# Optimization experiments

Measured on AMD Instinct MI355X. Metric: run time of the kernel, lower is better.

## Reference

```python
import jax, jax.numpy as jnp
import numpy as np

D_MODEL = 1024
NUM_HEADS = 16
D_K = D_MODEL // NUM_HEADS
B, S = 2, 2048


def setup_inputs() -> dict:
    key = jax.random.key(0)
    ks = jax.random.split(key, 11)
    s = 1.0 / np.sqrt(D_MODEL)
    inp = {
        "Q": jax.random.normal(ks[0], (B, S, D_MODEL), jnp.float32),
        "K": jax.random.normal(ks[1], (B, S, D_MODEL), jnp.float32),
        "V": jax.random.normal(ks[2], (B, S, D_MODEL), jnp.float32),
        "Wq": jax.random.uniform(ks[3], (D_MODEL, D_MODEL), jnp.float32, -s, s),
        "bq": jax.random.uniform(ks[4], (D_MODEL,), jnp.float32, -s, s),
        "Wk": jax.random.uniform(ks[5], (D_MODEL, D_MODEL), jnp.float32, -s, s),
        "bk": jax.random.uniform(ks[6], (D_MODEL,), jnp.float32, -s, s),
        "Wv": jax.random.uniform(ks[7], (D_MODEL, D_MODEL), jnp.float32, -s, s),
        "bv": jax.random.uniform(ks[8], (D_MODEL,), jnp.float32, -s, s),
        "Wo": jax.random.uniform(ks[9], (D_MODEL, D_MODEL), jnp.float32, -s, s),
        "bo": jax.random.uniform(ks[10], (D_MODEL,), jnp.float32, -s, s),
    }
    return inp


def _split_heads(x):
    b, s, _ = x.shape
    return x.reshape(b, s, NUM_HEADS, D_K).transpose(0, 2, 1, 3)  # [B,H,S,Dk]


def reference(Q, K, V, Wq, bq, Wk, bk, Wv, bv, Wo, bo):
    q = _split_heads(Q @ Wq.T + bq)
    k = _split_heads(K @ Wk.T + bk)
    v = _split_heads(V @ Wv.T + bv)
    scale = 1.0 / jnp.sqrt(jnp.asarray(D_K, q.dtype))
    scores = jnp.einsum("bhqd,bhkd->bhqk", q, k) * scale  # [B,H,S,S]
    attn = jax.nn.softmax(scores, axis=-1)
    out = jnp.einsum("bhqk,bhkd->bhqd", attn, v)
    out = out.transpose(0, 2, 1, 3).reshape(Q.shape[0], -1, D_MODEL)
    return out @ Wo.T + bo
```

## Files before the change

kernel.cpp:

```cpp
#include <hip/hip_runtime.h>
#include <stdint.h>

typedef __bf16 bf16;
typedef __bf16 bf16x8 __attribute__((ext_vector_type(8)));
typedef float floatx4 __attribute__((ext_vector_type(4)));

#define S_LEN 2048
#define DM 1024
#define NH 16
#define DK 64
#define MTOT 4096

__device__ __forceinline__ void gll16(const void* g, void* l) {
  __builtin_amdgcn_global_load_lds(
      (const __attribute__((address_space(1))) void*)g,
      (__attribute__((address_space(3))) void*)l, 16, 0, 0);
}

__global__ __launch_bounds__(256) void cvt_kernel(
    const float* __restrict__ Wq, const float* __restrict__ Wk, const float* __restrict__ Wv,
    const float* __restrict__ Xq, const float* __restrict__ Xk,
    bf16* __restrict__ wqb, bf16* __restrict__ wkb, bf16* __restrict__ wvb,
    bf16* __restrict__ xqb, bf16* __restrict__ xkb)
{
  const int c = blockIdx.x;
  const float* src; bf16* dst; int off;
  if      (c < 512)  { src = Wq; dst = wqb; off = c; }
  else if (c < 1024) { src = Wk; dst = wkb; off = c - 512; }
  else if (c < 1536) { src = Wv; dst = wvb; off = c - 1024; }
  else if (c < 3584) { src = Xq; dst = xqb; off = c - 1536; }
  else               { src = Xk; dst = xkb; off = c - 3584; }
  const size_t base = (size_t)off * 2048 + threadIdx.x * 8;
  float4 a = *(const float4*)(src + base);
  float4 b = *(const float4*)(src + base + 4);
  bf16x8 h;
  h[0] = (bf16)a.x; h[1] = (bf16)a.y; h[2] = (bf16)a.z; h[3] = (bf16)a.w;
  h[4] = (bf16)b.x; h[5] = (bf16)b.y; h[6] = (bf16)b.z; h[7] = (bf16)b.w;
  *(bf16x8*)(dst + base) = h;
}

__global__ __launch_bounds__(256) void proj_kernel(
    const bf16* __restrict__ xqb, const bf16* __restrict__ xkb, const float* __restrict__ Xv,
    const bf16* __restrict__ wqb, const bf16* __restrict__ wkb, const bf16* __restrict__ wvb,
    const float* __restrict__ bqp, const float* __restrict__ bkp, const float* __restrict__ bvp,
    bf16* __restrict__ qb, bf16* __restrict__ kb, bf16* __restrict__ vtb)
{
  const int z = blockIdx.z;
  const bf16* W     = (z == 0) ? wqb : (z == 1) ? wkb : wvb;
  const float* bias = (z == 0) ? bqp : (z == 1) ? bkp : bvp;

  const int m0 = blockIdx.x * 128;
  const int n0 = blockIdx.y * 128;
  const int tid = threadIdx.x;
  const int lane = tid & 63;
  const int wid = tid >> 6;
  const int wm = (wid & 1) * 64;
  const int wn = (wid >> 1) * 64;

  __shared__ unsigned char smemA[32768];
  __shared__ bf16 Bs[128 * 64];
  bf16*  As16 = (bf16*)smemA;
  float* Asf  = (float*)smemA;

  floatx4 acc[4][4];
  #pragma unroll
  for (int i = 0; i < 4; i++)
    #pragma unroll
    for (int j = 0; j < 4; j++) acc[i][j] = (floatx4){0.f, 0.f, 0.f, 0.f};

  const int mr = lane & 15;
  const int q4 = lane >> 4;

  const int r8_in = lane >> 3, cb8_ph = lane & 7;
  const int r4_in = lane >> 4, cb16_ph = lane & 15;

  const bf16* Xb = (z == 0) ? xqb : xkb;

  for (int kt = 0; kt < DM; kt += 64) {
    __syncthreads();
    if (z < 2) {
      #pragma unroll
      for (int j = 0; j < 4; j++) {
        const int c = wid * 4 + j;
        const int row = c * 8 + r8_in;
        const int cb = cb8_ph ^ (row & 7);
        gll16(Xb + (size_t)(m0 + row) * DM + kt + cb * 8, &As16[c * 512]);
      }
    } else {
      #pragma unroll
      for (int j = 0; j < 8; j++) {
        const int c = wid * 8 + j;
        const int row = c * 4 + r4_in;
        const int cb = cb16_ph ^ (row & 7);
        gll16(Xv + (size_t)(m0 + row) * DM + kt + cb * 4, &Asf[c * 256]);
      }
    }
    #pragma unroll
    for (int j = 0; j < 4; j++) {
      const int c = wid * 4 + j;
      const int row = c * 8 + r8_in;
      const int cb = cb8_ph ^ (row & 7);
      gll16(W + (size_t)(n0 + row) * DM + kt + cb * 8, &Bs[c * 512]);
    }
    __syncthreads();

    #pragma unroll
    for (int kk = 0; kk < 2; kk++) {
      bf16x8 af[4], bfr[4];
      #pragma unroll
      for (int mt = 0; mt < 4; mt++) {
        const int row = wm + mt * 16 + mr;
        if (z < 2) {
          const int cb = 4 * kk + q4;
          af[mt] = *(const bf16x8*)&As16[row * 64 + (cb ^ (row & 7)) * 8];
        } else {
          const int cb0 = 8 * kk + 2 * q4;
          const float4 lo = *(const float4*)&Asf[row * 64 + (cb0 ^ (row & 7)) * 4];
          const float4 hi = *(const float4*)&Asf[row * 64 + ((cb0 + 1) ^ (row & 7)) * 4];
          bf16x8 a;
          a[0] = (bf16)lo.x; a[1] = (bf16)lo.y; a[2] = (bf16)lo.z; a[3] = (bf16)lo.w;
          a[4] = (bf16)hi.x; a[5] = (bf16)hi.y; a[6] = (bf16)hi.z; a[7] = (bf16)hi.w;
          af[mt] = a;
        }
      }
      #pragma unroll
      for (int nt = 0; nt < 4; nt++) {
        const int row = wn + nt * 16 + mr;
        const int cb = 4 * kk + q4;
        bfr[nt] = *(const bf16x8*)&Bs[row * 64 + (cb ^ (row & 7)) * 8];
      }
      #pragma unroll
      for (int mt = 0; mt < 4; mt++)
        #pragma unroll
        for (int nt = 0; nt < 4; nt++)
          acc[mt][nt] = __builtin_amdgcn_mfma_f32_16x16x32_bf16(af[mt], bfr[nt], acc[mt][nt], 0, 0, 0);
    }
  }

  const float qscale = (z == 0) ? 0.125f : 1.0f;
  #pragma unroll
  for (int nt = 0; nt < 4; nt++) {
    const int gn = n0 + wn + nt * 16 + mr;
    const float bv = bias[gn];
    const int h = gn >> 6, d = gn & 63;
    #pragma unroll
    for (int mt = 0; mt < 4; mt++) {
      const int mbase = m0 + wm + mt * 16 + q4 * 4;
      #pragma unroll
      for (int r = 0; r < 4; r++) {
        const int gm = mbase + r;
        const int bi = gm >> 11, s = gm & 2047;
        const bf16 hv = (bf16)((acc[mt][nt][r] + bv) * qscale);
        if (z == 2) {
          vtb[(((size_t)(bi * NH + h)) * DK + d) * S_LEN + s] = hv;
        } else if (z == 0) {
          qb[(((size_t)(bi * NH + h)) * S_LEN + s) * DK + d] = hv;
        } else {
          kb[(((size_t)(bi * NH + h)) * S_LEN + s) * DK + d] = hv;
        }
      }
    }
  }
}

__global__ __launch_bounds__(256) void attn_kernel(
    const bf16* __restrict__ qb, const bf16* __restrict__ kb,
    const bf16* __restrict__ vtb, bf16* __restrict__ ob)
{
  const int qt = blockIdx.x;
  const int bh = blockIdx.y;
  const int tid = threadIdx.x;
  const int lane = tid & 63;
  const int wid = tid >> 6;

  const bf16* qh = qb + (size_t)bh * S_LEN * DK;
  const bf16* kh = kb + (size_t)bh * S_LEN * DK;
  const bf16* vh = vtb + (size_t)bh * DK * S_LEN;

  __shared__ bf16 Ks[128 * 64];
  __shared__ bf16 Vs[64 * 128];
  __shared__ bf16 Ps[4][32][136];

  const int mr = lane & 15;
  const int q4 = lane >> 4;

  bf16x8 aq[2][2];
  #pragma unroll
  for (int mt = 0; mt < 2; mt++)
    #pragma unroll
    for (int kk = 0; kk < 2; kk++)
      aq[mt][kk] = *(const bf16x8*)(qh + (size_t)(qt * 128 + wid * 32 + mt * 16 + mr) * DK + kk * 32 + q4 * 8);

  floatx4 acc_o[2][4];
  #pragma unroll
  for (int mt = 0; mt < 2; mt++)
    #pragma unroll
    for (int dt = 0; dt < 4; dt++) acc_o[mt][dt] = (floatx4){0.f, 0.f, 0.f, 0.f};
  float l_p[2][4] = {{0.f,0.f,0.f,0.f},{0.f,0.f,0.f,0.f}};

  const int r8_in = lane >> 3, cb8_ph = lane & 7;
  const int r4_in = lane >> 4, cb16_ph = lane & 15;

  for (int it = 0; it < S_LEN / 128; it++) {
    const int s0 = it * 128;
    __syncthreads();
    #pragma unroll
    for (int j = 0; j < 4; j++) {
      const int c = wid * 4 + j;
      const int row = c * 8 + r8_in;
      const int cb = cb8_ph ^ (row & 7);
      gll16(kh + (size_t)(s0 + row) * DK + cb * 8, &Ks[c * 512]);
    }
    #pragma unroll
    for (int j = 0; j < 4; j++) {
      const int c = wid * 4 + j;
      const int row = c * 4 + r4_in;
      const int cb = cb16_ph ^ (row & 7);
      gll16(vh + (size_t)row * S_LEN + s0 + cb * 8, &Vs[c * 512]);
    }
    __syncthreads();

    floatx4 sc[2][8];
    #pragma unroll
    for (int mt = 0; mt < 2; mt++)
      #pragma unroll
      for (int i = 0; i < 8; i++) sc[mt][i] = (floatx4){0.f, 0.f, 0.f, 0.f};
    #pragma unroll
    for (int kk = 0; kk < 2; kk++) {
      #pragma unroll
      for (int nt = 0; nt < 8; nt++) {
        const int row = nt * 16 + mr;
        const int cb = kk * 4 + q4;
        bf16x8 b = *(const bf16x8*)&Ks[row * 64 + (cb ^ (row & 7)) * 8];
        #pragma unroll
        for (int mt = 0; mt < 2; mt++)
          sc[mt][nt] = __builtin_amdgcn_mfma_f32_16x16x32_bf16(aq[mt][kk], b, sc[mt][nt], 0, 0, 0);
      }
    }

    #pragma unroll
    for (int mt = 0; mt < 2; mt++)
      #pragma unroll
      for (int nt = 0; nt < 8; nt++)
        #pragma unroll
        for (int r = 0; r < 4; r++) {
          const float pv = __expf(sc[mt][nt][r]);
          l_p[mt][r] += pv;
          Ps[wid][mt * 16 + q4 * 4 + r][nt * 16 + mr] = (bf16)pv;
        }

    #pragma unroll
    for (int kk2 = 0; kk2 < 4; kk2++) {
      bf16x8 ap[2];
      #pragma unroll
      for (int mt = 0; mt < 2; mt++)
        ap[mt] = *(const bf16x8*)&Ps[wid][mt * 16 + mr][kk2 * 32 + q4 * 8];
      #pragma unroll
      for (int dt = 0; dt < 4; dt++) {
        const int row = dt * 16 + mr;
        const int cb = kk2 * 4 + q4;
        bf16x8 b = *(const bf16x8*)&Vs[row * 128 + (cb ^ (row & 7)) * 8];
        #pragma unroll
        for (int mt = 0; mt < 2; mt++)
          acc_o[mt][dt] = __builtin_amdgcn_mfma_f32_16x16x32_bf16(ap[mt], b, acc_o[mt][dt], 0, 0, 0);
      }
    }
  }

  const int bi = bh >> 4, h = bh & 15;
  #pragma unroll
  for (int mt = 0; mt < 2; mt++) {
    float inv[4];
    #pragma unroll
    for (int r = 0; r < 4; r++) {
      float v = l_p[mt][r];
      #pragma unroll
      for (int off = 1; off < 16; off <<= 1) v += __shfl_xor(v, off, 16);
      inv[r] = 1.0f / v;
    }
    #pragma unroll
    for (int dt = 0; dt < 4; dt++) {
      const int d = dt * 16 + mr;
      #pragma unroll
      for (int r = 0; r < 4; r++) {
        const int s = qt * 128 + wid * 32 + mt * 16 + q4 * 4 + r;
        ob[((size_t)(bi * S_LEN + s)) * DM + h * DK + d] = (bf16)(acc_o[mt][dt][r] * inv[r]);
      }
    }
  }
}

__global__ __launch_bounds__(256) void oproj_kernel(
    const bf16* __restrict__ X, const float* __restrict__ W,
    const float* __restrict__ bias, float* __restrict__ out)
{
  const int m0 = blockIdx.x * 128;
  const int n0 = blockIdx.y * 64;
  const int tid = threadIdx.x;
  const int lane = tid & 63;
  const int wid = tid >> 6;
  const int wm = wid * 32;

  __shared__ bf16  As[128 * 64];
  __shared__ float Bsf[64 * 64];

  floatx4 acc[2][4];
  #pragma unroll
  for (int i = 0; i < 2; i++)
    #pragma unroll
    for (int j = 0; j < 4; j++) acc[i][j] = (floatx4){0.f, 0.f, 0.f, 0.f};

  const int mr = lane & 15;
  const int q4 = lane >> 4;

  const int r8_in = lane >> 3, cb8_ph = lane & 7;
  const int r4_in = lane >> 4, cb16_ph = lane & 15;

  for (int kt = 0; kt < DM; kt += 64) {
    __syncthreads();
    #pragma unroll
    for (int j = 0; j < 4; j++) {
      const int c = wid * 4 + j;
      const int row = c * 8 + r8_in;
      const int cb = cb8_ph ^ (row & 7);
      gll16(X + (size_t)(m0 + row) * DM + kt + cb * 8, &As[c * 512]);
    }
    #pragma unroll
    for (int j = 0; j < 4; j++) {
      const int c = wid * 4 + j;
      const int row = c * 4 + r4_in;
      const int cb = cb16_ph ^ (row & 7);
      gll16(W + (size_t)(n0 + row) * DM + kt + cb * 4, &Bsf[c * 256]);
    }
    __syncthreads();

    #pragma unroll
    for (int kk = 0; kk < 2; kk++) {
      bf16x8 af[2], bfr[4];
      #pragma unroll
      for (int mt = 0; mt < 2; mt++) {
        const int row = wm + mt * 16 + mr;
        const int cb = 4 * kk + q4;
        af[mt] = *(const bf16x8*)&As[row * 64 + (cb ^ (row & 7)) * 8];
      }
      #pragma unroll
      for (int nt = 0; nt < 4; nt++) {
        const int row = nt * 16 + mr;
        const int cb0 = 8 * kk + 2 * q4;
        const float4 lo = *(const float4*)&Bsf[row * 64 + (cb0 ^ (row & 7)) * 4];
        const float4 hi = *(const float4*)&Bsf[row * 64 + ((cb0 + 1) ^ (row & 7)) * 4];
        bf16x8 b;
        b[0] = (bf16)lo.x; b[1] = (bf16)lo.y; b[2] = (bf16)lo.z; b[3] = (bf16)lo.w;
        b[4] = (bf16)hi.x; b[5] = (bf16)hi.y; b[6] = (bf16)hi.z; b[7] = (bf16)hi.w;
        bfr[nt] = b;
      }
      #pragma unroll
      for (int mt = 0; mt < 2; mt++)
        #pragma unroll
        for (int nt = 0; nt < 4; nt++)
          acc[mt][nt] = __builtin_amdgcn_mfma_f32_16x16x32_bf16(af[mt], bfr[nt], acc[mt][nt], 0, 0, 0);
    }
  }

  #pragma unroll
  for (int nt = 0; nt < 4; nt++) {
    const int gn = n0 + nt * 16 + mr;
    const float bv = bias[gn];
    #pragma unroll
    for (int mt = 0; mt < 2; mt++) {
      const int mbase = m0 + wm + mt * 16 + q4 * 4;
      #pragma unroll
      for (int r = 0; r < 4; r++)
        out[(size_t)(mbase + r) * DM + gn] = acc[mt][nt][r] + bv;
    }
  }
}

extern "C" void kernel_launch(void* const* d_in, const int* in_sizes, int n_in,
                              void* d_out, int out_size, void* d_ws, size_t ws_size,
                              hipStream_t stream) {
  const float* Q  = (const float*)d_in[0];
  const float* K  = (const float*)d_in[1];
  const float* V  = (const float*)d_in[2];
  const float* Wq = (const float*)d_in[3];
  const float* bq = (const float*)d_in[4];
  const float* Wk = (const float*)d_in[5];
  const float* bk = (const float*)d_in[6];
  const float* Wv = (const float*)d_in[7];
  const float* bv = (const float*)d_in[8];
  const float* Wo = (const float*)d_in[9];
  const float* bo = (const float*)d_in[10];
  float* out = (float*)d_out;

  const size_t NE = (size_t)MTOT * DM;
  bf16* qb  = (bf16*)d_ws;
  bf16* kb  = qb + NE;
  bf16* vtb = kb + NE;
  bf16* ao  = vtb + NE;
  bf16* wqb = ao;
  bf16* wkb = ao + (size_t)DM * DM;
  bf16* wvb = ao + 2 * (size_t)DM * DM;
  bf16* xqb = (bf16*)d_out;
  bf16* xkb = xqb + NE;

  cvt_kernel<<<dim3(5632), 256, 0, stream>>>(Wq, Wk, Wv, Q, K, wqb, wkb, wvb, xqb, xkb);
  proj_kernel<<<dim3(32, 8, 3), 256, 0, stream>>>(xqb, xkb, V, wqb, wkb, wvb, bq, bk, bv, qb, kb, vtb);
  attn_kernel<<<dim3(16, 32), 256, 0, stream>>>(qb, kb, vtb, ao);
  oproj_kernel<<<dim3(32, 16), 256, 0, stream>>>(ao, Wo, bo, out);
}
```

Baseline: 262.8 us.

## Split proj kernel paths by input type and deepen oproj K tile

The projection kernel now runs separate K loops for the bf16 Q/K inputs (K-step 64) and the fp32 V input (K-step 32). This halves the shared-memory A buffer and removes the per-iteration branch on z. The output projection kernel doubles its K tile to 128, with wider XOR swizzles, so it runs half as many barrier-separated load phases. The trade-off is more shared memory per block in oproj (64KB), which may reduce occupancy, and more loop iterations for the V projection.

```diff
diff --git a/kernel.cpp b/kernel.cpp
--- a/kernel.cpp
+++ b/kernel.cpp
@@ -57,7 +57,7 @@
   const int wm = (wid & 1) * 64;
   const int wn = (wid >> 1) * 64;
 
-  __shared__ unsigned char smemA[32768];
+  __shared__ unsigned char smemA[16384];
   __shared__ bf16 Bs[128 * 64];
   bf16*  As16 = (bf16*)smemA;
   float* Asf  = (float*)smemA;
@@ -72,13 +72,12 @@
   const int q4 = lane >> 4;
 
   const int r8_in = lane >> 3, cb8_ph = lane & 7;
-  const int r4_in = lane >> 4, cb16_ph = lane & 15;
-
-  const bf16* Xb = (z == 0) ? xqb : xkb;
-
-  for (int kt = 0; kt < DM; kt += 64) {
-    __syncthreads();
-    if (z < 2) {
+  const int r16_in = lane >> 2, cb4_ph = lane & 3;
+
+  if (z < 2) {
+    const bf16* Xb = (z == 0) ? xqb : xkb;
+    for (int kt = 0; kt < DM; kt += 64) {
+      __syncthreads();
       #pragma unroll
       for (int j = 0; j < 4; j++) {
         const int c = wid * 4 + j;
@@ -86,48 +85,72 @@
         const int cb = cb8_ph ^ (row & 7);
         gll16(Xb + (size_t)(m0 + row) * DM + kt + cb * 8, &As16[c * 512]);
       }
-    } else {
-      #pragma unroll
-      for (int j = 0; j < 8; j++) {
-        const int c = wid * 8 + j;
-        const int row = c * 4 + r4_in;
-        const int cb = cb16_ph ^ (row & 7);
+      #pragma unroll
+      for (int j = 0; j < 4; j++) {
+        const int c = wid * 4 + j;
+        const int row = c * 8 + r8_in;
+        const int cb = cb8_ph ^ (row & 7);
+        gll16(W + (size_t)(n0 + row) * DM + kt + cb * 8, &Bs[c * 512]);
+      }
+      __syncthreads();
+
+      #pragma unroll
+      for (int kk = 0; kk < 2; kk++) {
+        bf16x8 af[4], bfr[4];
+        #pragma unroll
+        for (int mt = 0; mt < 4; mt++) {
+          const int row = wm + mt * 16 + mr;
+          const int cb = 4 * kk + q4;
+          af[mt] = *(const bf16x8*)&As16[row * 64 + (cb ^ (row & 7)) * 8];
+        }
+        #pragma unroll
+        for (int nt = 0; nt < 4; nt++) {
+          const int row = wn + nt * 16 + mr;
+          const int cb = 4 * kk + q4;
+          bfr[nt] = *(const bf16x8*)&Bs[row * 64 + (cb ^ (row & 7)) * 8];
+        }
+        #pragma unroll
+        for (int mt = 0; mt < 4; mt++)
+          #pragma unroll
+          for (int nt = 0; nt < 4; nt++)
+            acc[mt][nt] = __builtin_amdgcn_mfma_f32_16x16x32_bf16(af[mt], bfr[nt], acc[mt][nt], 0, 0, 0);
+      }
+    }
+  } else {
+    for (int kt = 0; kt < DM; kt += 32) {
+      __syncthreads();
+      #pragma unroll
+      for (int j = 0; j < 4; j++) {
+        const int c = wid * 4 + j;
+        const int row = c * 8 + r8_in;
+        const int cb = cb8_ph ^ (row & 7);
         gll16(Xv + (size_t)(m0 + row) * DM + kt + cb * 4, &Asf[c * 256]);
       }
-    }
-    #pragma unroll
-    for (int j = 0; j < 4; j++) {
-      const int c = wid * 4 + j;
-      const int row = c * 8 + r8_in;
-      const int cb = cb8_ph ^ (row & 7);
-      gll16(W + (size_t)(n0 + row) * DM + kt + cb * 8, &Bs[c * 512]);
-    }
-    __syncthreads();
-
-    #pragma unroll
-    for (int kk = 0; kk < 2; kk++) {
+      #pragma unroll
+      for (int j = 0; j < 2; j++) {
+        const int c = wid * 2 + j;
+        const int row = c * 16 + r16_in;
+        const int cb = cb4_ph ^ (row & 3);
+        gll16(W + (size_t)(n0 + row) * DM + kt + cb * 8, &Bs[c * 512]);
+      }
+      __syncthreads();
+
       bf16x8 af[4], bfr[4];
       #pragma unroll
       for (int mt = 0; mt < 4; mt++) {
         const int row = wm + mt * 16 + mr;
-        if (z < 2) {
-          const int cb = 4 * kk + q4;
-          af[mt] = *(const bf16x8*)&As16[row * 64 + (cb ^ (row & 7)) * 8];
-        } else {
-          const int cb0 = 8 * kk + 2 * q4;
-          const float4 lo = *(const float4*)&Asf[row * 64 + (cb0 ^ (row & 7)) * 4];
-          const float4 hi = *(const float4*)&Asf[row * 64 + ((cb0 + 1) ^ (row & 7)) * 4];
-          bf16x8 a;
-          a[0] = (bf16)lo.x; a[1] = (bf16)lo.y; a[2] = (bf16)lo.z; a[3] = (bf16)lo.w;
-          a[4] = (bf16)hi.x; a[5] = (bf16)hi.y; a[6] = (bf16)hi.z; a[7] = (bf16)hi.w;
-          af[mt] = a;
-        }
+        const int cb0 = 2 * q4;
+        const float4 lo = *(const float4*)&Asf[row * 32 + (cb0 ^ (row & 7)) * 4];
+        const float4 hi = *(const float4*)&Asf[row * 32 + ((cb0 + 1) ^ (row & 7)) * 4];
+        bf16x8 a;
+        a[0] = (bf16)lo.x; a[1] = (bf16)lo.y; a[2] = (bf16)lo.z; a[3] = (bf16)lo.w;
+        a[4] = (bf16)hi.x; a[5] = (bf16)hi.y; a[6] = (bf16)hi.z; a[7] = (bf16)hi.w;
+        af[mt] = a;
       }
       #pragma unroll
       for (int nt = 0; nt < 4; nt++) {
         const int row = wn + nt * 16 + mr;
-        const int cb = 4 * kk + q4;
-        bfr[nt] = *(const bf16x8*)&Bs[row * 64 + (cb ^ (row & 7)) * 8];
+        bfr[nt] = *(const bf16x8*)&Bs[row * 32 + (q4 ^ (row & 3)) * 8];
       }
       #pragma unroll
       for (int mt = 0; mt < 4; mt++)
@@ -301,8 +324,8 @@
   const int wid = tid >> 6;
   const int wm = wid * 32;
 
-  __shared__ bf16  As[128 * 64];
-  __shared__ float Bsf[64 * 64];
+  __shared__ bf16  As[128 * 128];
+  __shared__ float Bsf[64 * 128];
 
   floatx4 acc[2][4];
   #pragma unroll
@@ -313,42 +336,42 @@
   const int mr = lane & 15;
   const int q4 = lane >> 4;
 
-  const int r8_in = lane >> 3, cb8_ph = lane & 7;
   const int r4_in = lane >> 4, cb16_ph = lane & 15;
-
-  for (int kt = 0; kt < DM; kt += 64) {
+  const int r2_in = lane >> 5, cb32_ph = lane & 31;
+
+  for (int kt = 0; kt < DM; kt += 128) {
     __syncthreads();
     #pragma unroll
-    for (int j = 0; j < 4; j++) {
-      const int c = wid * 4 + j;
-      const int row = c * 8 + r8_in;
-      const int cb = cb8_ph ^ (row & 7);
+    for (int j = 0; j < 8; j++) {
+      const int c = wid * 8 + j;
+      const int row = c * 4 + r4_in;
+      const int cb = cb16_ph ^ (row & 15);
       gll16(X + (size_t)(m0 + row) * DM + kt + cb * 8, &As[c * 512]);
     }
     #pragma unroll
-    for (int j = 0; j < 4; j++) {
-      const int c = wid * 4 + j;
-      const int row = c * 4 + r4_in;
-      const int cb = cb16_ph ^ (row & 7);
+    for (int j = 0; j < 8; j++) {
+      const int c = wid * 8 + j;
+      const int row = c * 2 + r2_in;
+      const int cb = cb32_ph ^ (row & 31);
       gll16(W + (size_t)(n0 + row) * DM + kt + cb * 4, &Bsf[c * 256]);
     }
     __syncthreads();
 
     #pragma unroll
-    for (int kk = 0; kk < 2; kk++) {
+    for (int kk = 0; kk < 4; kk++) {
       bf16x8 af[2], bfr[4];
       #pragma unroll
       for (int mt = 0; mt < 2; mt++) {
         const int row = wm + mt * 16 + mr;
         const int cb = 4 * kk + q4;
-        af[mt] = *(const bf16x8*)&As[row * 64 + (cb ^ (row & 7)) * 8];
+        af[mt] = *(const bf16x8*)&As[row * 128 + (cb ^ (row & 15)) * 8];
       }
       #pragma unroll
       for (int nt = 0; nt < 4; nt++) {
         const int row = nt * 16 + mr;
         const int cb0 = 8 * kk + 2 * q4;
-        const float4 lo = *(const float4*)&Bsf[row * 64 + (cb0 ^ (row & 7)) * 4];
-        const float4 hi = *(const float4*)&Bsf[row * 64 + ((cb0 + 1) ^ (row & 7)) * 4];
+        const float4 lo = *(const float4*)&Bsf[row * 128 + (cb0 ^ (row & 31)) * 4];
+        const float4 hi = *(const float4*)&Bsf[row * 128 + ((cb0 + 1) ^ (row & 31)) * 4];
         bf16x8 b;
         b[0] = (bf16)lo.x; b[1] = (bf16)lo.y; b[2] = (bf16)lo.z; b[3] = (bf16)lo.w;
         b[4] = (bf16)hi.x; b[5] = (bf16)hi.y; b[6] = (bf16)hi.z; b[7] = (bf16)hi.w;
```

Measured after the change: 270.8 us. +3.0%, slower.
